# Optimization experiments

Hardware: AMD Instinct MI355X
Metric: run time of the kernel (lower is better)

Reference implementation:

```python
import jax, jax.numpy as jnp
import numpy as np

B, L, D = 2, 4096, 1024
H, HD = 16, D // 16
W = 256          # window_size
C = 256          # chunk/block size (== W, so each block sees prev + current block)
NC = L // C
SCALE = HD ** -0.5


def complex_linear(z, Wr, Wi):
    # z: [..., D, 2]; W*: [out, in] (torch Linear convention y = x @ W^T)
    xr, xi = z[..., 0], z[..., 1]
    yr = jnp.einsum('...i,oi->...o', xr, Wr) - jnp.einsum('...i,oi->...o', xi, Wi)
    yi = jnp.einsum('...i,oi->...o', xr, Wi) + jnp.einsum('...i,oi->...o', xi, Wr)
    return jnp.stack([yr, yi], axis=-1)


def _heads(x):
    # [B, L, D, 2] -> [B, H, NC, C, HD, 2]
    return x.reshape(B, L, H, HD, 2).transpose(0, 2, 1, 3, 4).reshape(B, H, NC, C, HD, 2)


def _band_mask():
    # block c, query local qi (global i = c*C + qi), key local kj over [prev block | cur block]
    # global j = (c-1)*C + kj ; valid iff 0 <= j <= i and i - j < W
    c = jnp.arange(NC)[:, None, None]
    qi = jnp.arange(C)[None, :, None]
    kj = jnp.arange(2 * C)[None, None, :]
    i = c * C + qi
    j = (c - 1) * C + kj
    return (j >= 0) & (j <= i) & (i - j < W)  # [NC, C, 2C]


def setup_inputs() -> dict:
    key = jax.random.key(0)
    ks = jax.random.split(key, 9)
    s = D ** -0.5
    inp = {'z': jax.random.normal(ks[0], (B, L, D, 2), jnp.float32)}
    names = ['Wq_r', 'Wq_i', 'Wk_r', 'Wk_i', 'Wv_r', 'Wv_i', 'Wo_r', 'Wo_i']
    for n, k in zip(names, ks[1:]):
        inp[n] = jax.random.normal(k, (D, D), jnp.float32) * s
    return inp


def reference(z, Wq_r, Wq_i, Wk_r, Wk_i, Wv_r, Wv_i, Wo_r, Wo_i):
    q = _heads(complex_linear(z, Wq_r, Wq_i))  # [B,H,NC,C,HD,2]
    k = _heads(complex_linear(z, Wk_r, Wk_i))
    v = _heads(complex_linear(z, Wv_r, Wv_i))

    def with_prev(x):  # [B,H,NC,C,HD,2] -> [B,H,NC,2C,HD,2] (prev block | cur block)
        prev = jnp.concatenate([jnp.zeros_like(x[:, :, :1]), x[:, :, :-1]], axis=2)
        return jnp.concatenate([prev, x], axis=3)

    kc = with_prev(k)
    vc = with_prev(v)

    # Re(q * conj(k)) = qr*kr + qi*ki
    scores = (jnp.einsum('bhncd,bhnkd->bhnck', q[..., 0], kc[..., 0])
              + jnp.einsum('bhncd,bhnkd->bhnck', q[..., 1], kc[..., 1])) * SCALE
    scores = jnp.where(_band_mask()[None, None], scores, -jnp.inf)
    w = jax.nn.softmax(scores, axis=-1)  # [B,H,NC,C,2C]

    out_r = jnp.einsum('bhnck,bhnkd->bhncd', w, vc[..., 0])
    out_i = jnp.einsum('bhnck,bhnkd->bhncd', w, vc[..., 1])
    out = jnp.stack([out_r, out_i], axis=-1)           # [B,H,NC,C,HD,2]
    out = out.reshape(B, H, L, HD, 2).transpose(0, 2, 1, 3, 4).reshape(B, L, D, 2)
    return complex_linear(out, Wo_r, Wo_i)
```

## Files before the change

### kernel.cpp

```cpp
#include <hip/hip_runtime.h>
#include <hip/hip_bf16.h>
#include <stdint.h>


typedef __attribute__((ext_vector_type(8))) short bf16x8;
typedef __attribute__((ext_vector_type(4))) float f32x4;

#define PA_SCALE 0.125f
#define UNR _Pragma("unroll")

__device__ __forceinline__ unsigned short f2bf(float f) {
  unsigned int u = __builtin_bit_cast(unsigned int, f);
  u += 0x7fffu + ((u >> 16) & 1u);
  return (unsigned short)(u >> 16);
}

#define GLD16(gp, lp)                                          \
  __builtin_amdgcn_global_load_lds(                            \
      (const __attribute__((address_space(1))) void*)(gp),     \
      (__attribute__((address_space(3))) void*)(lp), 16, 0, 0)

__global__ __launch_bounds__(256) void pa_pack_A(const float* __restrict__ z,
                                                 unsigned short* __restrict__ A1) {
  int idx = blockIdx.x * 256 + threadIdx.x;
  float2 f = ((const float2*)z)[idx];
  int m = idx >> 10, d = idx & 1023;
  size_t base = (size_t)m * 2048 + d;
  A1[base]        = f2bf(f.x);
  A1[base + 1024] = f2bf(f.y);
}

__global__ __launch_bounds__(256) void pa_pack_B(
    const float* __restrict__ Wq_r, const float* __restrict__ Wq_i,
    const float* __restrict__ Wk_r, const float* __restrict__ Wk_i,
    const float* __restrict__ Wv_r, const float* __restrict__ Wv_i,
    const float* __restrict__ Wo_r, const float* __restrict__ Wo_i,
    unsigned short* __restrict__ Bp) {
  int idx = blockIdx.x * 256 + threadIdx.x;
  int n = idx >> 10, d = idx & 1023;
  int proj = n >> 11, part = (n >> 10) & 1, o = n & 1023;
  const float* Wr; const float* Wi;
  if (proj == 0)      { Wr = Wq_r; Wi = Wq_i; }
  else if (proj == 1) { Wr = Wk_r; Wi = Wk_i; }
  else if (proj == 2) { Wr = Wv_r; Wi = Wv_i; }
  else                { Wr = Wo_r; Wi = Wo_i; }
  float r  = Wr[(size_t)o * 1024 + d];
  float im = Wi[(size_t)o * 1024 + d];
  size_t base = (size_t)n * 2048 + d;
  if (part == 0) { Bp[base] = f2bf(r);  Bp[base + 1024] = f2bf(-im); }
  else           { Bp[base] = f2bf(im); Bp[base + 1024] = f2bf(r);  }
}

#define BARR()                              \
  do {                                      \
    __builtin_amdgcn_s_barrier();           \
    __builtin_amdgcn_sched_barrier(0);      \
  } while (0)

#define READ_A(P, MH)                                                         \
  UNR for (int i = 0; i < 4; ++i)                                             \
    UNR for (int ks = 0; ks < 2; ++ks)                                        \
      af[i][ks] = *(const bf16x8*)&lds[P][MH][aoff + i * 1024 +               \
                                              ((ks * 32 + koff) ^ cxor)];

#define READ_B(P, NH, DST)                                                    \
  UNR for (int j = 0; j < 2; ++j)                                             \
    UNR for (int ks = 0; ks < 2; ++ks)                                        \
      DST[j][ks] = *(const bf16x8*)&lds[P][2 + (NH)][boff + j * 1024 +        \
                                                     ((ks * 32 + koff) ^ cxor)];

#define MFMA_Q(MB, NB, BF)                                                    \
  UNR for (int ks = 0; ks < 2; ++ks)                                          \
    UNR for (int i = 0; i < 4; ++i)                                           \
      UNR for (int j = 0; j < 2; ++j)                                         \
        acc[(MB) + i][(NB) + j] = __builtin_amdgcn_mfma_f32_16x16x32_bf16(    \
            af[i][ks], BF[j][ks], acc[(MB) + i][(NB) + j], 0, 0, 0);

#define TILE(P, T)                                                            \
  {                                                                           \
    READ_A(P, 0);                                                             \
    READ_B(P, 0, b0);                                                         \
    stageB(0, (T) + 1);                                                       \
    BARR();                                                                   \
    __builtin_amdgcn_s_setprio(1);                                            \
    MFMA_Q(0, 0, b0);                                                         \
    __builtin_amdgcn_s_setprio(0);                                            \
    BARR();                                                                   \
    READ_B(P, 1, b1);                                                         \
    stageA(0, (T) + 2);                                                       \
    BARR();                                                                   \
    __builtin_amdgcn_s_setprio(1);                                            \
    MFMA_Q(0, 2, b1);                                                         \
    __builtin_amdgcn_s_setprio(0);                                            \
    BARR();                                                                   \
    READ_A(P, 1);                                                             \
    stageB(1, (T) + 2);                                                       \
    BARR();                                                                   \
    __builtin_amdgcn_s_setprio(1);                                            \
    MFMA_Q(4, 2, b1);                                                         \
    __builtin_amdgcn_s_setprio(0);                                            \
    BARR();                                                                   \
    stageA(1, (T) + 2);                                                       \
    BARR();                                                                   \
    __builtin_amdgcn_s_setprio(1);                                            \
    MFMA_Q(4, 0, b0);                                                         \
    __builtin_amdgcn_s_setprio(0);                                            \
    asm volatile("s_waitcnt vmcnt(6)" ::: "memory");                          \
    __builtin_amdgcn_sched_barrier(0);                                        \
    BARR();                                                                   \
  }

template <int EPI>
__global__ __launch_bounds__(512, 2) void pa_gemm8(
    const unsigned short* __restrict__ A,
    const unsigned short* __restrict__ B,
    void* __restrict__ Cout, int K, int N) {
  __shared__ unsigned short lds[2][4][128 * 64];

  const int tid = threadIdx.x;
  const int lane = tid & 63, wid = tid >> 6;
  const int wm = wid >> 2, wn = wid & 3;
  const int lr = lane & 15, lh = lane >> 4;

  const int nwg = gridDim.x * gridDim.y;
  const int wg = blockIdx.y * gridDim.x + blockIdx.x;
  const int cpx = nwg >> 3;
  const int swz = (wg & 7) * cpx + (wg >> 3);
  const int bx = swz % gridDim.x, by = swz / gridDim.x;
  const int tm0 = by * 256, tn0 = bx * 256;

  const int NT = K >> 6;

  const int srow = lane >> 3;
  const int scolS = ((lane & 7) ^ srow) * 8;

  auto stageA = [&](int half, int ts) {
    int t = ts < NT ? ts : ts - NT;
    const unsigned short* g0 = A + (size_t)(tm0 + half * 128) * K + t * 64 + scolS;
    unsigned short* l0 = &lds[ts & 1][half][0];
    UNR for (int c = 0; c < 2; ++c) {
      int chunk = wid * 2 + c;
      GLD16(g0 + (size_t)(chunk * 8 + srow) * K, l0 + chunk * 512);
    }
  };
  auto stageB = [&](int half, int ts) {
    int t = ts < NT ? ts : ts - NT;
    const unsigned short* g0 = B + (size_t)(tn0 + half * 128) * K + t * 64 + scolS;
    unsigned short* l0 = &lds[ts & 1][2 + half][0];
    UNR for (int c = 0; c < 2; ++c) {
      int chunk = wid * 2 + c;
      GLD16(g0 + (size_t)(chunk * 8 + srow) * K, l0 + chunk * 512);
    }
  };

  const int aoff = (wm * 64 + lr) * 64;
  const int boff = (wn * 32 + lr) * 64;
  const int koff = lh * 8;
  const int cxor = (lr & 7) * 8;

  f32x4 acc[8][4];
  f32x4 zero4 = {0.f, 0.f, 0.f, 0.f};
  UNR for (int i = 0; i < 8; ++i)
    UNR for (int j = 0; j < 4; ++j) acc[i][j] = zero4;

  bf16x8 af[4][2], b0[2][2], b1[2][2];

  stageA(0, 0); stageB(0, 0); stageB(1, 0); stageA(1, 0);
  stageA(0, 1); stageB(1, 1); stageA(1, 1);
  asm volatile("s_waitcnt vmcnt(6)" ::: "memory");
  __builtin_amdgcn_sched_barrier(0);
  __builtin_amdgcn_s_barrier();
  __builtin_amdgcn_sched_barrier(0);

  for (int t = 0; t < NT; t += 2) {
    TILE(0, t);
    TILE(1, t + 1);
  }

  UNR for (int mh = 0; mh < 2; ++mh)
    UNR for (int i = 0; i < 4; ++i)
      UNR for (int nh = 0; nh < 2; ++nh)
        UNR for (int j = 0; j < 2; ++j)
          UNR for (int r = 0; r < 4; ++r) {
            int row = tm0 + mh * 128 + wm * 64 + i * 16 + lh * 4 + r;
            int col = tn0 + nh * 128 + wn * 32 + j * 16 + lr;
            float v = acc[mh * 4 + i][nh * 2 + j][r];
            if (EPI == 0) {
              ((unsigned short*)Cout)[(size_t)row * N + col] = f2bf(v);
            } else {
              int part = col >> 10, dd = col & 1023;
              ((float*)Cout)[((size_t)row * 1024 + dd) * 2 + part] = v;
            }
          }
}

__global__ __launch_bounds__(256) void pa_attn(const unsigned short* __restrict__ C1,
                                               unsigned short* __restrict__ A2) {
  __shared__ unsigned short Ks[2][64][72];
  __shared__ unsigned short Vts[2][64][72];
  __shared__ unsigned short Ps[4][16][72];

  int bid = blockIdx.x;
  int qq = bid & 3, nc = (bid >> 2) & 15, h = (bid >> 6) & 15, b = bid >> 10;
  int tid = threadIdx.x;
  int l = tid & 63, wv = tid >> 6;
  int lr = l & 15, lh = l >> 4;

  const int C1LD = 6144;
  const int rowB = b * 4096;
  const int colQr = h * 64,        colQi = 1024 + h * 64;
  const int colKr = 2048 + h * 64, colKi = 3072 + h * 64;
  const int colVr = 4096 + h * 64, colVi = 5120 + h * 64;
  const int q0 = qq * 64;
  const int qw = q0 + wv * 16;

  bf16x8 qfr[2], qfi[2];
  {
    const unsigned short* pr = C1 + (size_t)(rowB + nc * 256 + qw + lr) * C1LD + colQr;
    const unsigned short* pi = C1 + (size_t)(rowB + nc * 256 + qw + lr) * C1LD + colQi;
    qfr[0] = *(const bf16x8*)(pr + lh * 8);
    qfr[1] = *(const bf16x8*)(pr + 32 + lh * 8);
    qfi[0] = *(const bf16x8*)(pi + lh * 8);
    qfi[1] = *(const bf16x8*)(pi + 32 + lh * 8);
  }

  f32x4 zero4 = {0.f, 0.f, 0.f, 0.f};
  f32x4 sac[5][4];
#pragma unroll
  for (int c = 0; c < 5; ++c)
#pragma unroll
    for (int f = 0; f < 4; ++f) sac[c][f] = zero4;

#pragma unroll
  for (int c = 0; c < 5; ++c) {
    __syncthreads();
#pragma unroll
    for (int s = 0; s < 4; ++s) {
      int seg = s * 256 + tid;
      int arr = seg >> 9, row = (seg >> 3) & 63, sg = seg & 7;
      int kj = q0 + c * 64 + row;
      int tok = (nc - 1) * 256 + kj; if (tok < 0) tok = 0;
      const unsigned short* src =
          C1 + (size_t)(rowB + tok) * C1LD + (arr ? colKi : colKr) + sg * 8;
      *(bf16x8*)&Ks[arr][row][sg * 8] = *(const bf16x8*)src;
    }
    __syncthreads();
#pragma unroll
    for (int kk = 0; kk < 2; ++kk) {
#pragma unroll
      for (int f = 0; f < 4; ++f) {
        bf16x8 br = *(const bf16x8*)&Ks[0][f * 16 + lr][kk * 32 + lh * 8];
        bf16x8 bi = *(const bf16x8*)&Ks[1][f * 16 + lr][kk * 32 + lh * 8];
        sac[c][f] = __builtin_amdgcn_mfma_f32_16x16x32_bf16(qfr[kk], br, sac[c][f], 0, 0, 0);
        sac[c][f] = __builtin_amdgcn_mfma_f32_16x16x32_bf16(qfi[kk], bi, sac[c][f], 0, 0, 0);
      }
    }
  }

  float mx[4] = {-1e30f, -1e30f, -1e30f, -1e30f};
#pragma unroll
  for (int c = 0; c < 5; ++c)
#pragma unroll
    for (int f = 0; f < 4; ++f)
#pragma unroll
      for (int r = 0; r < 4; ++r) {
        int qi_ = qw + lh * 4 + r;
        int kj  = q0 + c * 64 + f * 16 + lr;
        bool valid = (kj > qi_) && (kj <= qi_ + 256) && (nc > 0 || kj >= 256);
        float s = valid ? sac[c][f][r] * PA_SCALE : -1e30f;
        sac[c][f][r] = s;
        mx[r] = fmaxf(mx[r], s);
      }
#pragma unroll
  for (int r = 0; r < 4; ++r)
#pragma unroll
    for (int d = 1; d < 16; d <<= 1) mx[r] = fmaxf(mx[r], __shfl_xor(mx[r], d));

  float sm[4] = {0.f, 0.f, 0.f, 0.f};
#pragma unroll
  for (int c = 0; c < 5; ++c)
#pragma unroll
    for (int f = 0; f < 4; ++f)
#pragma unroll
      for (int r = 0; r < 4; ++r) {
        float p = __expf(sac[c][f][r] - mx[r]);
        sac[c][f][r] = p;
        sm[r] += p;
      }
#pragma unroll
  for (int r = 0; r < 4; ++r)
#pragma unroll
    for (int d = 1; d < 16; d <<= 1) sm[r] += __shfl_xor(sm[r], d);
  float inv[4];
#pragma unroll
  for (int r = 0; r < 4; ++r) inv[r] = 1.0f / sm[r];

  f32x4 oac[2][4];
#pragma unroll
  for (int p = 0; p < 2; ++p)
#pragma unroll
    for (int f = 0; f < 4; ++f) oac[p][f] = zero4;

#pragma unroll
  for (int c = 0; c < 5; ++c) {
    __syncthreads();
#pragma unroll
    for (int s = 0; s < 4; ++s) {
      int seg = s * 256 + tid;
      int arr = seg >> 9, row = (seg >> 3) & 63, sg = seg & 7;
      int kj = q0 + c * 64 + row;
      int tok = (nc - 1) * 256 + kj; if (tok < 0) tok = 0;
      const unsigned short* src =
          C1 + (size_t)(rowB + tok) * C1LD + (arr ? colVi : colVr) + sg * 8;
      bf16x8 v = *(const bf16x8*)src;
#pragma unroll
      for (int j = 0; j < 8; ++j) Vts[arr][sg * 8 + j][row] = (unsigned short)v[j];
    }
#pragma unroll
    for (int f = 0; f < 4; ++f)
#pragma unroll
      for (int r = 0; r < 4; ++r)
        Ps[wv][lh * 4 + r][f * 16 + lr] = f2bf(sac[c][f][r]);
    __syncthreads();

    bf16x8 pa0 = *(const bf16x8*)&Ps[wv][lr][lh * 8];
    bf16x8 pa1 = *(const bf16x8*)&Ps[wv][lr][32 + lh * 8];
#pragma unroll
    for (int kk = 0; kk < 2; ++kk) {
      bf16x8 pak = kk ? pa1 : pa0;
#pragma unroll
      for (int fc = 0; fc < 4; ++fc) {
        bf16x8 vr = *(const bf16x8*)&Vts[0][fc * 16 + lr][kk * 32 + lh * 8];
        bf16x8 vi = *(const bf16x8*)&Vts[1][fc * 16 + lr][kk * 32 + lh * 8];
        oac[0][fc] = __builtin_amdgcn_mfma_f32_16x16x32_bf16(pak, vr, oac[0][fc], 0, 0, 0);
        oac[1][fc] = __builtin_amdgcn_mfma_f32_16x16x32_bf16(pak, vi, oac[1][fc], 0, 0, 0);
      }
    }
  }

#pragma unroll
  for (int fc = 0; fc < 4; ++fc)
#pragma unroll
    for (int r = 0; r < 4; ++r) {
      int m  = rowB + nc * 256 + qw + lh * 4 + r;
      int hd = fc * 16 + lr;
      A2[(size_t)m * 2048 + h * 64 + hd]        = f2bf(oac[0][fc][r] * inv[r]);
      A2[(size_t)m * 2048 + 1024 + h * 64 + hd] = f2bf(oac[1][fc][r] * inv[r]);
    }
}

extern "C" void kernel_launch(void* const* d_in, const int* in_sizes, int n_in,
                              void* d_out, int out_size, void* d_ws, size_t ws_size,
                              hipStream_t stream) {
  const float* z = (const float*)d_in[0];
  unsigned short* A1 = (unsigned short*)d_ws;
  unsigned short* Bp = (unsigned short*)((char*)d_ws + 33554432ull);
  unsigned short* C1 = (unsigned short*)((char*)d_ws + 67108864ull);
  float* out = (float*)d_out;

  pa_pack_A<<<32768, 256, 0, stream>>>(z, A1);
  pa_pack_B<<<32768, 256, 0, stream>>>(
      (const float*)d_in[1], (const float*)d_in[2],
      (const float*)d_in[3], (const float*)d_in[4],
      (const float*)d_in[5], (const float*)d_in[6],
      (const float*)d_in[7], (const float*)d_in[8], Bp);
  pa_gemm8<0><<<dim3(24, 32), 512, 0, stream>>>(A1, Bp, C1, 2048, 6144);
  pa_attn<<<2048, 256, 0, stream>>>(C1, A1);
  pa_gemm8<1><<<dim3(8, 32), 512, 0, stream>>>(A1, Bp + (size_t)6144 * 2048, out,
                                               2048, 2048);
}
```

Measured before the change: 390.5 us.

## Vectorize pack kernels and reorder GEMM tile pipeline with prefetched A fragments

The pack kernels now have each thread convert 8 consecutive elements and write 16-byte vectors, with the grids shrunk to match, which cuts scalar 2-byte stores and launch granularity. The GEMM main loop is reordered so the next tile's A and B fragments are read from LDS during the current tile. Ping-pong A register buffers are added, and vmcnt waits are placed after each MFMA quarter. This aims to hide LDS and global load latency better but raises register pressure, which matters under launch_bounds(512,2).

```diff
diff --git a/kernel.cpp b/kernel.cpp
--- a/kernel.cpp
+++ b/kernel.cpp
@@ -4,6 +4,7 @@
 
 
 typedef __attribute__((ext_vector_type(8))) short bf16x8;
+typedef __attribute__((ext_vector_type(8))) unsigned short u16x8;
 typedef __attribute__((ext_vector_type(4))) float f32x4;
 
 #define PA_SCALE 0.125f
@@ -22,12 +23,17 @@
 
 __global__ __launch_bounds__(256) void pa_pack_A(const float* __restrict__ z,
                                                  unsigned short* __restrict__ A1) {
-  int idx = blockIdx.x * 256 + threadIdx.x;
-  float2 f = ((const float2*)z)[idx];
+  int idx = (blockIdx.x * 256 + threadIdx.x) * 8;
   int m = idx >> 10, d = idx & 1023;
-  size_t base = (size_t)m * 2048 + d;
-  A1[base]        = f2bf(f.x);
-  A1[base + 1024] = f2bf(f.y);
+  const float2* zp = (const float2*)z + idx;
+  u16x8 re, im;
+  UNR for (int j = 0; j < 8; ++j) {
+    float2 f = zp[j];
+    re[j] = f2bf(f.x);
+    im[j] = f2bf(f.y);
+  }
+  *(u16x8*)(A1 + (size_t)m * 2048 + d)        = re;
+  *(u16x8*)(A1 + (size_t)m * 2048 + 1024 + d) = im;
 }
 
 __global__ __launch_bounds__(256) void pa_pack_B(
@@ -36,7 +42,7 @@
     const float* __restrict__ Wv_r, const float* __restrict__ Wv_i,
     const float* __restrict__ Wo_r, const float* __restrict__ Wo_i,
     unsigned short* __restrict__ Bp) {
-  int idx = blockIdx.x * 256 + threadIdx.x;
+  int idx = (blockIdx.x * 256 + threadIdx.x) * 8;
   int n = idx >> 10, d = idx & 1023;
   int proj = n >> 11, part = (n >> 10) & 1, o = n & 1023;
   const float* Wr; const float* Wi;
@@ -44,11 +50,16 @@
   else if (proj == 1) { Wr = Wk_r; Wi = Wk_i; }
   else if (proj == 2) { Wr = Wv_r; Wi = Wv_i; }
   else                { Wr = Wo_r; Wi = Wo_i; }
-  float r  = Wr[(size_t)o * 1024 + d];
-  float im = Wi[(size_t)o * 1024 + d];
-  size_t base = (size_t)n * 2048 + d;
-  if (part == 0) { Bp[base] = f2bf(r);  Bp[base + 1024] = f2bf(-im); }
-  else           { Bp[base] = f2bf(im); Bp[base + 1024] = f2bf(r);  }
+  const float* pr = Wr + (size_t)o * 1024 + d;
+  const float* pi = Wi + (size_t)o * 1024 + d;
+  u16x8 lo, hi;
+  UNR for (int j = 0; j < 8; ++j) {
+    float r = pr[j], im = pi[j];
+    if (part == 0) { lo[j] = f2bf(r);  hi[j] = f2bf(-im); }
+    else           { lo[j] = f2bf(im); hi[j] = f2bf(r);  }
+  }
+  *(u16x8*)(Bp + (size_t)n * 2048 + d)        = lo;
+  *(u16x8*)(Bp + (size_t)n * 2048 + 1024 + d) = hi;
 }
 
 #define BARR()                              \
@@ -57,11 +68,17 @@
     __builtin_amdgcn_sched_barrier(0);      \
   } while (0)
 
-#define READ_A(P, MH)                                                         \
+#define VMC6()                                                \
+  do {                                                        \
+    asm volatile("s_waitcnt vmcnt(6)" ::: "memory");          \
+    __builtin_amdgcn_sched_barrier(0);                        \
+  } while (0)
+
+#define READ_A(P, MH, DST)                                                    \
   UNR for (int i = 0; i < 4; ++i)                                             \
     UNR for (int ks = 0; ks < 2; ++ks)                                        \
-      af[i][ks] = *(const bf16x8*)&lds[P][MH][aoff + i * 1024 +               \
-                                              ((ks * 32 + koff) ^ cxor)];
+      DST[i][ks] = *(const bf16x8*)&lds[P][MH][aoff + i * 1024 +              \
+                                               ((ks * 32 + koff) ^ cxor)];
 
 #define READ_B(P, NH, DST)                                                    \
   UNR for (int j = 0; j < 2; ++j)                                             \
@@ -69,44 +86,46 @@
       DST[j][ks] = *(const bf16x8*)&lds[P][2 + (NH)][boff + j * 1024 +        \
                                                      ((ks * 32 + koff) ^ cxor)];
 
-#define MFMA_Q(MB, NB, BF)                                                    \
+#define MFMA_Q(MB, NB, AF, BF)                                                \
   UNR for (int ks = 0; ks < 2; ++ks)                                          \
     UNR for (int i = 0; i < 4; ++i)                                           \
       UNR for (int j = 0; j < 2; ++j)                                         \
         acc[(MB) + i][(NB) + j] = __builtin_amdgcn_mfma_f32_16x16x32_bf16(    \
-            af[i][ks], BF[j][ks], acc[(MB) + i][(NB) + j], 0, 0, 0);
-
-#define TILE(P, T)                                                            \
+            AF[i][ks], BF[j][ks], acc[(MB) + i][(NB) + j], 0, 0, 0);
+
+#define TILE(P, T, AF0, AF0N)                                                 \
   {                                                                           \
-    READ_A(P, 0);                                                             \
-    READ_B(P, 0, b0);                                                         \
-    stageB(0, (T) + 1);                                                       \
+    READ_A(P, 1, af1);                                                        \
+    stageA(1, (T) + 1);                                                       \
     BARR();                                                                   \
     __builtin_amdgcn_s_setprio(1);                                            \
-    MFMA_Q(0, 0, b0);                                                         \
+    MFMA_Q(0, 0, AF0, b0);                                                    \
     __builtin_amdgcn_s_setprio(0);                                            \
+    VMC6();                                                                   \
     BARR();                                                                   \
     READ_B(P, 1, b1);                                                         \
+    stageB(1, (T) + 1);                                                       \
+    BARR();                                                                   \
+    __builtin_amdgcn_s_setprio(1);                                            \
+    MFMA_Q(4, 0, af1, b0);                                                    \
+    __builtin_amdgcn_s_setprio(0);                                            \
+    VMC6();                                                                   \
+    BARR();                                                                   \
+    READ_A((P) ^ 1, 0, AF0N);                                                 \
     stageA(0, (T) + 2);                                                       \
     BARR();                                                                   \
     __builtin_amdgcn_s_setprio(1);                                            \
-    MFMA_Q(0, 2, b1);                                                         \
+    MFMA_Q(4, 2, af1, b1);                                                    \
     __builtin_amdgcn_s_setprio(0);                                            \
-    BARR();                                                                   \
-    READ_A(P, 1);                                                             \
-    stageB(1, (T) + 2);                                                       \
+    VMC6();                                                                   \
+    BARR();                                                                   \
+    READ_B((P) ^ 1, 0, b0);                                                   \
+    stageB(0, (T) + 2);                                                       \
     BARR();                                                                   \
     __builtin_amdgcn_s_setprio(1);                                            \
-    MFMA_Q(4, 2, b1);                                                         \
+    MFMA_Q(0, 2, AF0, b1);                                                    \
     __builtin_amdgcn_s_setprio(0);                                            \
-    BARR();                                                                   \
-    stageA(1, (T) + 2);                                                       \
-    BARR();                                                                   \
-    __builtin_amdgcn_s_setprio(1);                                            \
-    MFMA_Q(4, 0, b0);                                                         \
-    __builtin_amdgcn_s_setprio(0);                                            \
-    asm volatile("s_waitcnt vmcnt(6)" ::: "memory");                          \
-    __builtin_amdgcn_sched_barrier(0);                                        \
+    VMC6();                                                                   \
     BARR();                                                                   \
   }
 
@@ -163,18 +182,19 @@
   UNR for (int i = 0; i < 8; ++i)
     UNR for (int j = 0; j < 4; ++j) acc[i][j] = zero4;
 
-  bf16x8 af[4][2], b0[2][2], b1[2][2];
-
-  stageA(0, 0); stageB(0, 0); stageB(1, 0); stageA(1, 0);
-  stageA(0, 1); stageB(1, 1); stageA(1, 1);
-  asm volatile("s_waitcnt vmcnt(6)" ::: "memory");
-  __builtin_amdgcn_sched_barrier(0);
+  bf16x8 af0a[4][2], af0b[4][2], af1[4][2], b0[2][2], b1[2][2];
+
+  stageA(0, 0); stageB(0, 0); stageA(1, 0); stageB(1, 0);
+  stageA(0, 1); stageB(0, 1);
+  VMC6();
   __builtin_amdgcn_s_barrier();
   __builtin_amdgcn_sched_barrier(0);
+  READ_A(0, 0, af0a);
+  READ_B(0, 0, b0);
 
   for (int t = 0; t < NT; t += 2) {
-    TILE(0, t);
-    TILE(1, t + 1);
+    TILE(0, t, af0a, af0b);
+    TILE(1, t + 1, af0b, af0a);
   }
 
   UNR for (int mh = 0; mh < 2; ++mh)
@@ -358,8 +378,8 @@
   unsigned short* C1 = (unsigned short*)((char*)d_ws + 67108864ull);
   float* out = (float*)d_out;
 
-  pa_pack_A<<<32768, 256, 0, stream>>>(z, A1);
-  pa_pack_B<<<32768, 256, 0, stream>>>(
+  pa_pack_A<<<4096, 256, 0, stream>>>(z, A1);
+  pa_pack_B<<<4096, 256, 0, stream>>>(
       (const float*)d_in[1], (const float*)d_in[2],
       (const float*)d_in[3], (const float*)d_in[4],
       (const float*)d_in[5], (const float*)d_in[6],
```

New measurement: 942.8 us. 141% more time.
